# Performance work log

Measured on AMD Instinct MI355X. Metric: run time of the kernel, lower is better.

## Reference

```python
import jax, jax.numpy as jnp
import numpy as np

DENSITY_FACTOR = 1.0
WHITE_BACKGROUND = False
FAR_DELTA = 1e4
EPS_DIST = 1e-5
EPS_ALPHA = 1e-8

N_RAYS = 65536
N_SAMPLES = 192
C_RGB = 3


def setup_inputs() -> dict:
    key = jax.random.key(0)
    k1, k2 = jax.random.split(key)
    rgba = jax.random.normal(k1, (N_RAYS, N_SAMPLES, C_RGB + 1), dtype=jnp.float32)
    # distances along each ray, sorted ascending (realistic sample depths in [0, 4))
    distance = jnp.sort(4.0 * jax.random.uniform(k2, (N_RAYS, N_SAMPLES), dtype=jnp.float32), axis=-1)
    return {"rgba": rgba, "distance": distance}


def reference(rgba, distance):
    # over_opacity_extra from hyperreel TensorReduce
    rgb = jax.nn.sigmoid(rgba[..., :-1])          # [N, S, C]
    density = rgba[..., -1]                        # [N, S]
    density = jnp.where(distance < EPS_DIST, jnp.zeros_like(density), density)
    density = jax.nn.relu(density) * DENSITY_FACTOR
    # deltas between consecutive samples; last delta is "infinite" (1e4)
    deltas = jnp.concatenate(
        [jnp.abs(distance[:, 1:] - distance[:, :-1]),
         FAR_DELTA * jnp.ones_like(distance[:, :1])], axis=1)
    alpha = 1.0 - jnp.exp(-deltas * density)       # [N, S]
    # over_composite_one: transmittance via exclusive cumprod of (1 - alpha)
    alphas_shifted = jnp.concatenate(
        [jnp.ones_like(alpha[:, :1]), 1.0 - alpha + EPS_ALPHA], axis=-1)
    trans = jnp.cumprod(alphas_shifted, axis=-1)[:, :-1]   # [N, S]
    weights = alpha * trans                                 # [N, S]
    rgb_final = jnp.einsum('ns,nsc->nc', weights, rgb)      # [N, C]
    if WHITE_BACKGROUND:
        accum = weights.sum(-1)
        rgb_final = rgb_final + (1.0 - accum[..., None])
    return rgb_final
```

## Files before the change

kernel.cpp:

```cpp
#include <hip/hip_runtime.h>
#include <math.h>

#define N_RAYS    65536
#define N_SAMPLES 192
#define FAR_DELTA 1e4f
#define EPS_DIST  1e-5f
#define EPS_ALPHA 1e-8f

typedef float floatx4 __attribute__((ext_vector_type(4)));

__global__ __launch_bounds__(256) void composite_kernel(
    const float* __restrict__ rgba,
    const float* __restrict__ dist,
    float* __restrict__ out)
{
    const int lane = threadIdx.x & 63;
    const int ray  = blockIdx.x * 4 + (threadIdx.x >> 6);

    const floatx4* __restrict__ rgba4 =
        (const floatx4*)rgba + (size_t)ray * N_SAMPLES + lane * 3;
    const float* __restrict__ d =
        dist + (size_t)ray * N_SAMPLES + lane * 3;

    floatx4 v0 = __builtin_nontemporal_load(rgba4 + 0);
    floatx4 v1 = __builtin_nontemporal_load(rgba4 + 1);
    floatx4 v2 = __builtin_nontemporal_load(rgba4 + 2);
    float d0 = __builtin_nontemporal_load(d + 0);
    float d1 = __builtin_nontemporal_load(d + 1);
    float d2 = __builtin_nontemporal_load(d + 2);
    float d3 = __shfl_down(d0, 1, 64);

    float dl0 = fabsf(d1 - d0);
    float dl1 = fabsf(d2 - d1);
    float dl2 = (lane == 63) ? FAR_DELTA : fabsf(d3 - d2);

    float den0 = (d0 < EPS_DIST) ? 0.0f : fmaxf(v0.w, 0.0f);
    float den1 = (d1 < EPS_DIST) ? 0.0f : fmaxf(v1.w, 0.0f);
    float den2 = (d2 < EPS_DIST) ? 0.0f : fmaxf(v2.w, 0.0f);

    float t0 = __expf(-dl0 * den0);
    float t1 = __expf(-dl1 * den1);
    float t2 = __expf(-dl2 * den2);

    float a0 = 1.0f - t0, a1 = 1.0f - t1, a2 = 1.0f - t2;
    float p0 = t0 + EPS_ALPHA, p1 = t1 + EPS_ALPHA, p2 = t2 + EPS_ALPHA;

    float e1 = p0;
    float e2 = p0 * p1;
    float Ltot = e2 * p2;

    float P = Ltot;
    #pragma unroll
    for (int off = 1; off < 64; off <<= 1) {
        float t = __shfl_up(P, off, 64);
        if (lane >= off) P *= t;
    }
    float E = __shfl_up(P, 1, 64);
    if (lane == 0) E = 1.0f;

    float w0 = a0 * E;
    float w1 = a1 * E * e1;
    float w2 = a2 * E * e2;

    float r_acc = w0 * __builtin_amdgcn_rcpf(1.0f + __expf(-v0.x))
                + w1 * __builtin_amdgcn_rcpf(1.0f + __expf(-v1.x))
                + w2 * __builtin_amdgcn_rcpf(1.0f + __expf(-v2.x));
    float g_acc = w0 * __builtin_amdgcn_rcpf(1.0f + __expf(-v0.y))
                + w1 * __builtin_amdgcn_rcpf(1.0f + __expf(-v1.y))
                + w2 * __builtin_amdgcn_rcpf(1.0f + __expf(-v2.y));
    float b_acc = w0 * __builtin_amdgcn_rcpf(1.0f + __expf(-v0.z))
                + w1 * __builtin_amdgcn_rcpf(1.0f + __expf(-v1.z))
                + w2 * __builtin_amdgcn_rcpf(1.0f + __expf(-v2.z));

    #pragma unroll
    for (int off = 32; off > 0; off >>= 1) {
        r_acc += __shfl_down(r_acc, off, 64);
        g_acc += __shfl_down(g_acc, off, 64);
        b_acc += __shfl_down(b_acc, off, 64);
    }

    if (lane == 0) {
        out[(size_t)ray * 3 + 0] = r_acc;
        out[(size_t)ray * 3 + 1] = g_acc;
        out[(size_t)ray * 3 + 2] = b_acc;
    }
}

extern "C" void kernel_launch(void* const* d_in, const int* in_sizes, int n_in,
                              void* d_out, int out_size, void* d_ws, size_t ws_size,
                              hipStream_t stream) {
    const float* rgba = (const float*)d_in[0];
    const float* dist = (const float*)d_in[1];
    float* out = (float*)d_out;

    dim3 grid(N_RAYS / 4);
    dim3 block(256);
    composite_kernel<<<grid, block, 0, stream>>>(rgba, dist, out);
}
```

Before: 289.7 us.

## Use strided sample-to-lane mapping for coalesced loads with three wave scans

Each lane now handles samples lane, lane+64 and lane+128 instead of three contiguous samples, so consecutive lanes read consecutive float4 and float addresses. The aim is fully coalesced, unit-stride memory accesses. In exchange the transmittance prefix product runs three 64-lane shuffle scans instead of one, plus extra broadcasts to chain the segments and fix up the boundary distances.

```diff
diff --git a/kernel.cpp b/kernel.cpp
--- a/kernel.cpp
+++ b/kernel.cpp
@@ -18,21 +18,27 @@
     const int ray  = blockIdx.x * 4 + (threadIdx.x >> 6);
 
     const floatx4* __restrict__ rgba4 =
-        (const floatx4*)rgba + (size_t)ray * N_SAMPLES + lane * 3;
+        (const floatx4*)rgba + (size_t)ray * N_SAMPLES + lane;
     const float* __restrict__ d =
-        dist + (size_t)ray * N_SAMPLES + lane * 3;
+        dist + (size_t)ray * N_SAMPLES + lane;
 
     floatx4 v0 = __builtin_nontemporal_load(rgba4 + 0);
-    floatx4 v1 = __builtin_nontemporal_load(rgba4 + 1);
-    floatx4 v2 = __builtin_nontemporal_load(rgba4 + 2);
+    floatx4 v1 = __builtin_nontemporal_load(rgba4 + 64);
+    floatx4 v2 = __builtin_nontemporal_load(rgba4 + 128);
     float d0 = __builtin_nontemporal_load(d + 0);
-    float d1 = __builtin_nontemporal_load(d + 1);
-    float d2 = __builtin_nontemporal_load(d + 2);
-    float d3 = __shfl_down(d0, 1, 64);
+    float d1 = __builtin_nontemporal_load(d + 64);
+    float d2 = __builtin_nontemporal_load(d + 128);
 
-    float dl0 = fabsf(d1 - d0);
-    float dl1 = fabsf(d2 - d1);
-    float dl2 = (lane == 63) ? FAR_DELTA : fabsf(d3 - d2);
+    float dn0 = __shfl_down(d0, 1, 64);
+    float dn1 = __shfl_down(d1, 1, 64);
+    float dn2 = __shfl_down(d2, 1, 64);
+    float b1  = __shfl(d1, 0, 64);
+    float b2  = __shfl(d2, 0, 64);
+    if (lane == 63) { dn0 = b1; dn1 = b2; }
+
+    float dl0 = fabsf(dn0 - d0);
+    float dl1 = fabsf(dn1 - d1);
+    float dl2 = (lane == 63) ? FAR_DELTA : fabsf(dn2 - d2);
 
     float den0 = (d0 < EPS_DIST) ? 0.0f : fmaxf(v0.w, 0.0f);
     float den1 = (d1 < EPS_DIST) ? 0.0f : fmaxf(v1.w, 0.0f);
@@ -43,24 +49,25 @@
     float t2 = __expf(-dl2 * den2);
 
     float a0 = 1.0f - t0, a1 = 1.0f - t1, a2 = 1.0f - t2;
-    float p0 = t0 + EPS_ALPHA, p1 = t1 + EPS_ALPHA, p2 = t2 + EPS_ALPHA;
+    float P0 = t0 + EPS_ALPHA, P1 = t1 + EPS_ALPHA, P2 = t2 + EPS_ALPHA;
 
-    float e1 = p0;
-    float e2 = p0 * p1;
-    float Ltot = e2 * p2;
-
-    float P = Ltot;
     #pragma unroll
     for (int off = 1; off < 64; off <<= 1) {
-        float t = __shfl_up(P, off, 64);
-        if (lane >= off) P *= t;
+        float s0 = __shfl_up(P0, off, 64);
+        float s1 = __shfl_up(P1, off, 64);
+        float s2 = __shfl_up(P2, off, 64);
+        if (lane >= off) { P0 *= s0; P1 *= s1; P2 *= s2; }
     }
-    float E = __shfl_up(P, 1, 64);
-    if (lane == 0) E = 1.0f;
+    float E0 = __shfl_up(P0, 1, 64);
+    float E1 = __shfl_up(P1, 1, 64);
+    float E2 = __shfl_up(P2, 1, 64);
+    if (lane == 0) { E0 = 1.0f; E1 = 1.0f; E2 = 1.0f; }
+    float T1 = __shfl(P0, 63, 64);
+    float T2 = T1 * __shfl(P1, 63, 64);
 
-    float w0 = a0 * E;
-    float w1 = a1 * E * e1;
-    float w2 = a2 * E * e2;
+    float w0 = a0 * E0;
+    float w1 = a1 * T1 * E1;
+    float w2 = a2 * T2 * E2;
 
     float r_acc = w0 * __builtin_amdgcn_rcpf(1.0f + __expf(-v0.x))
                 + w1 * __builtin_amdgcn_rcpf(1.0f + __expf(-v1.x))
```

Result: faster. 278.8 us (-3.8%).
